# Performance work log

Measured on AMD Instinct MI355X. Metric: run time of the kernel, lower is better.

The kernel has to match this reference:

```python
import jax, jax.numpy as jnp
import numpy as np

N_NODES = 50000
N_RAND_EDGES = 800000  # plus N_NODES self-loop edges appended in setup
IN_FEATS, N_HIDDEN, N_CLASSES = 128, 64, 64


def setup_inputs() -> dict:
    key = jax.random.key(0)
    kf, ks, kd, k1, k2, k3 = jax.random.split(key, 6)
    features = jax.random.normal(kf, (N_NODES, IN_FEATS), dtype=jnp.float32)
    src = jax.random.randint(ks, (N_RAND_EDGES,), 0, N_NODES, dtype=jnp.int32)
    dst = jax.random.randint(kd, (N_RAND_EDGES,), 0, N_NODES, dtype=jnp.int32)
    # dgl.add_self_loop: append (i, i) for every node
    loop = jnp.arange(N_NODES, dtype=jnp.int32)
    src = jnp.concatenate([src, loop])
    dst = jnp.concatenate([dst, loop])

    def glorot(k, fan_in, fan_out):
        lim = jnp.sqrt(6.0 / (fan_in + fan_out)).astype(jnp.float32)
        return jax.random.uniform(k, (fan_in, fan_out), jnp.float32, -lim, lim)

    return {
        "features": features, "src": src, "dst": dst,
        "W1": glorot(k1, IN_FEATS, N_HIDDEN), "b1": jnp.zeros((N_HIDDEN,), jnp.float32),
        "W2": glorot(k2, N_HIDDEN, N_HIDDEN), "b2": jnp.zeros((N_HIDDEN,), jnp.float32),
        "W3": glorot(k3, N_HIDDEN, N_CLASSES), "b3": jnp.zeros((N_CLASSES,), jnp.float32),
    }


def _graph_conv(x, W, b, src, dst, norm_src_e, norm_dst_n, n_nodes):
    """DGL GraphConv, norm='both': D_dst^{-1/2} A D_src^{-1/2} X W + b, then relu."""
    if W.shape[0] > W.shape[1]:  # mult by W first when it shrinks the feature dim
        x = x @ W
        m = x[src] * norm_src_e[:, None]                      # [E, out]
        h = jax.ops.segment_sum(m, dst, num_segments=n_nodes)  # [N, out]
        h = h * norm_dst_n[:, None]
    else:
        m = x[src] * norm_src_e[:, None]                      # [E, in]
        h = jax.ops.segment_sum(m, dst, num_segments=n_nodes)  # [N, in]
        h = (h * norm_dst_n[:, None]) @ W
    return jax.nn.relu(h + b)


def reference(features, src, dst, W1, b1, W2, b2, W3, b3):
    n = features.shape[0]
    ones = jnp.ones(src.shape[0], dtype=features.dtype)
    out_deg = jax.ops.segment_sum(ones, src, num_segments=n)
    in_deg = jax.ops.segment_sum(ones, dst, num_segments=n)
    norm_out = jnp.where(out_deg > 0, jax.lax.rsqrt(jnp.maximum(out_deg, 1.0)), 0.0)
    norm_in = jnp.where(in_deg > 0, jax.lax.rsqrt(jnp.maximum(in_deg, 1.0)), 0.0)
    norm_src_e = norm_out[src]  # per-edge source normalization

    h1 = _graph_conv(features, W1, b1, src, dst, norm_src_e, norm_in, n)
    h2 = _graph_conv(h1, W2, b2, src, dst, norm_src_e, norm_in, n)
    h3 = _graph_conv(h2, W3, b3, src, dst, norm_src_e, norm_in, n)
    # JumpingKnowledge mode='max': elementwise max over stacked layer outputs
    return jnp.max(jnp.stack([h1, h2, h3], axis=0), axis=0)
```

## Files before the change

kernel.cpp:

```cpp
#include <hip/hip_runtime.h>

typedef _Float16 h16;
typedef __attribute__((ext_vector_type(4))) _Float16 half4;
typedef __attribute__((ext_vector_type(8))) _Float16 half8;
typedef __attribute__((ext_vector_type(8))) float float8;

#define RANGES 4
#define PPR    64
#define HTHREADS 1024
#define BINS   12800
#define HALF   (BINS / 2)
#define HWORDS (BINS)
#define NSEG   100
#define NFILL  (RANGES * PPR)
#define SMEMB  (BINS * 4 + 512)

__global__ __launch_bounds__(HTHREADS) void hist_kernel(const int* __restrict__ src,
                                                        const int* __restrict__ dst,
                                                        int* __restrict__ partial, int E) {
  __shared__ int h[HWORDS];
  const int r = blockIdx.x >> 6;
  const int c = blockIdx.x & 63;
  for (int i = threadIdx.x; i < HWORDS; i += HTHREADS) h[i] = 0;
  __syncthreads();
  const int lo = r * BINS;
  const int chunk = (E + PPR - 1) / PPR;
  const int e0 = c * chunk;
  const int e1 = min(E, e0 + chunk);
  for (int e = e0 + threadIdx.x; e < e1; e += HTHREADS) {
    int s = src[e] - lo;
    if ((unsigned)s < (unsigned)BINS) atomicAdd(&h[s >> 1], 1 << ((s & 1) * 16));
    int d = dst[e] - lo;
    if ((unsigned)d < (unsigned)BINS) atomicAdd(&h[HALF + (d >> 1)], 1 << ((d & 1) * 16));
  }
  __syncthreads();
  int* op = partial + (size_t)blockIdx.x * HWORDS;
  for (int i = threadIdx.x; i < HWORDS; i += HTHREADS) op[i] = h[i];
}

__global__ __launch_bounds__(256) void reduce_norm_scan1(
    int* __restrict__ partial, float* __restrict__ nout, float* __restrict__ nin,
    int* __restrict__ rowptr, int* __restrict__ bsums, int N) {
  __shared__ int s[256];
  const int j = blockIdx.x * 256 + threadIdx.x;
  const int r = j / HALF;
  const int w = j % HALF;
  int* base = partial + (size_t)(r * PPR) * HWORDS;
  int sumO = 0, runI = 0;
#pragma unroll 8
  for (int p = 0; p < PPR; ++p) {
    sumO += base[(size_t)p * HWORDS + w];
    int vI = base[(size_t)p * HWORDS + HALF + w];
    base[(size_t)p * HWORDS + HALF + w] = runI;
    runI += vI;
  }
  const int od0 = sumO & 0xFFFF, od1 = (sumO >> 16) & 0xFFFF;
  const int id0 = runI & 0xFFFF, id1 = (runI >> 16) & 0xFFFF;
  const int n0 = 2 * j, n1 = n0 + 1;
  if (n0 < N) {
    nout[n0] = od0 > 0 ? rsqrtf((float)od0) : 0.f;
    nin[n0]  = id0 > 0 ? rsqrtf((float)id0) : 0.f;
  }
  if (n1 < N) {
    nout[n1] = od1 > 0 ? rsqrtf((float)od1) : 0.f;
    nin[n1]  = id1 > 0 ? rsqrtf((float)id1) : 0.f;
  }
  const int local = id0 + id1;
  int v = local;
  s[threadIdx.x] = v;
  __syncthreads();
#pragma unroll
  for (int off = 1; off < 256; off <<= 1) {
    int tv = 0;
    if (threadIdx.x >= off) tv = s[threadIdx.x - off];
    __syncthreads();
    if (threadIdx.x >= off) s[threadIdx.x] += tv;
    __syncthreads();
  }
  const int excl = s[threadIdx.x] - v;
  if (n0 < N) rowptr[n0] = excl;
  if (n1 < N) rowptr[n1] = excl + id0;
  if (threadIdx.x == 255) bsums[blockIdx.x] = s[255];
}

__global__ __launch_bounds__(HTHREADS) void fill_gemm_kernel(
    const int* __restrict__ src, const int* __restrict__ dst,
    const int* __restrict__ rowptr, const int* __restrict__ bsums,
    const int* __restrict__ partial, int* __restrict__ rowptr_abs,
    unsigned short* __restrict__ csr,
    const float* __restrict__ feat, const float* __restrict__ W1,
    const float* __restrict__ nout, half4* __restrict__ bufAh,
    int N, int E) {
  __shared__ __align__(16) char smem[SMEMB];
  const int tid = threadIdx.x;

  if (blockIdx.x < NFILL) {
    int* cur = (int*)smem;
    int* top = (int*)(smem + BINS * 4);
    const int r = blockIdx.x & 3;
    const int c = blockIdx.x >> 2;
    if (tid < 128) top[tid] = (tid < NSEG) ? bsums[tid] : 0;
    __syncthreads();
#pragma unroll
    for (int off = 1; off < 128; off <<= 1) {
      int v = 0;
      if (tid < 128 && tid >= off) v = top[tid - off];
      __syncthreads();
      if (tid < 128 && tid >= off) top[tid] += v;
      __syncthreads();
    }
    const int lo = r * BINS;
    const int* pf = partial + (size_t)(r * PPR + c) * HWORDS + HALF;
    for (int n = tid; n < BINS; n += HTHREADS) {
      int g = lo + n;
      int rp = 0;
      if (g < N) {
        int seg = g >> 9;
        rp = rowptr[g] + (seg ? top[seg - 1] : 0);
        if (c == 0) rowptr_abs[g] = rp;
      }
      int pw = pf[n >> 1];
      cur[n] = rp + ((pw >> ((n & 1) * 16)) & 0xFFFF);
    }
    if (blockIdx.x == 0 && tid == 0) rowptr_abs[N] = E;
    __syncthreads();
    const int chunk = (E + PPR - 1) / PPR;
    const int e0 = c * chunk;
    const int e1 = min(E, e0 + chunk);
    for (int e = e0 + tid; e < e1; e += HTHREADS) {
      int d = dst[e] - lo;
      if ((unsigned)d < (unsigned)BINS) {
        int pos = atomicAdd(&cur[d], 1);
        csr[pos] = (unsigned short)src[e];
      }
    }
  } else {
    float* sA = (float*)smem;
    float* sB = (float*)(smem + 128 * 68 * 4);
    const int tile = blockIdx.x - NFILL;
    const int row0 = tile << 7;
    const int ry = tid >> 4;
    const int tx = tid & 15;
    const int r0 = 2 * ry, r1 = r0 + 1;
    float4 acc0 = make_float4(0.f, 0.f, 0.f, 0.f);
    float4 acc1 = make_float4(0.f, 0.f, 0.f, 0.f);
#pragma unroll
    for (int kc = 0; kc < 2; ++kc) {
      __syncthreads();
      for (int i = tid * 4; i < 128 * 64; i += HTHREADS * 4) {
        int rr = i >> 6, cc = i & 63;
        int gr = row0 + rr;
        float4 v = make_float4(0.f, 0.f, 0.f, 0.f);
        if (gr < N) v = *reinterpret_cast<const float4*>(feat + (size_t)gr * 128 + kc * 64 + cc);
        *reinterpret_cast<float4*>(sA + rr * 68 + cc) = v;
      }
      {
        int i = tid * 4;
        int rr = i >> 6, cc = i & 63;
        *reinterpret_cast<float4*>(sB + rr * 64 + cc) =
            *reinterpret_cast<const float4*>(W1 + (size_t)(kc * 64 + rr) * 64 + cc);
      }
      __syncthreads();
#pragma unroll 8
      for (int k = 0; k < 64; ++k) {
        float a0 = sA[r0 * 68 + k], a1 = sA[r1 * 68 + k];
        float4 b = *reinterpret_cast<float4*>(sB + k * 64 + tx * 4);
        acc0.x += a0 * b.x; acc0.y += a0 * b.y; acc0.z += a0 * b.z; acc0.w += a0 * b.w;
        acc1.x += a1 * b.x; acc1.y += a1 * b.y; acc1.z += a1 * b.z; acc1.w += a1 * b.w;
      }
    }
#pragma unroll
    for (int rr = 0; rr < 2; ++rr) {
      const int gr = row0 + (rr ? r1 : r0);
      if (gr >= N) continue;
      float4 v = rr ? acc1 : acc0;
      float no = nout[gr];
      half4 hv;
      hv.x = (h16)(v.x * no); hv.y = (h16)(v.y * no);
      hv.z = (h16)(v.z * no); hv.w = (h16)(v.w * no);
      bufAh[(size_t)gr * 16 + tx] = hv;
    }
  }
}

__device__ __forceinline__ float8 gather_row(const int* __restrict__ rowptr,
                                             const unsigned short* __restrict__ csr,
                                             const half8* __restrict__ xv,
                                             int node, int lane) {
  const int b = rowptr[node], e = rowptr[node + 1];
  float8 a0 = 0.f, a1 = 0.f, a2 = 0.f, a3 = 0.f;
  int i = b;
  for (; i + 8 <= e; i += 8) {
    int s0 = csr[i + 0], s1 = csr[i + 1], s2 = csr[i + 2], s3 = csr[i + 3];
    int s4 = csr[i + 4], s5 = csr[i + 5], s6 = csr[i + 6], s7 = csr[i + 7];
    half8 v0 = xv[(size_t)s0 * 8 + lane];
    half8 v1 = xv[(size_t)s1 * 8 + lane];
    half8 v2 = xv[(size_t)s2 * 8 + lane];
    half8 v3 = xv[(size_t)s3 * 8 + lane];
    half8 v4 = xv[(size_t)s4 * 8 + lane];
    half8 v5 = xv[(size_t)s5 * 8 + lane];
    half8 v6 = xv[(size_t)s6 * 8 + lane];
    half8 v7 = xv[(size_t)s7 * 8 + lane];
#pragma unroll
    for (int j = 0; j < 8; ++j) {
      a0[j] += (float)v0[j]; a1[j] += (float)v1[j];
      a2[j] += (float)v2[j]; a3[j] += (float)v3[j];
      a0[j] += (float)v4[j]; a1[j] += (float)v5[j];
      a2[j] += (float)v6[j]; a3[j] += (float)v7[j];
    }
  }
  for (; i + 4 <= e; i += 4) {
    int s0 = csr[i + 0], s1 = csr[i + 1], s2 = csr[i + 2], s3 = csr[i + 3];
    half8 v0 = xv[(size_t)s0 * 8 + lane];
    half8 v1 = xv[(size_t)s1 * 8 + lane];
    half8 v2 = xv[(size_t)s2 * 8 + lane];
    half8 v3 = xv[(size_t)s3 * 8 + lane];
#pragma unroll
    for (int j = 0; j < 8; ++j) {
      a0[j] += (float)v0[j]; a1[j] += (float)v1[j];
      a2[j] += (float)v2[j]; a3[j] += (float)v3[j];
    }
  }
  for (; i < e; ++i) {
    int s = csr[i];
    half8 v = xv[(size_t)s * 8 + lane];
#pragma unroll
    for (int j = 0; j < 8; ++j) a0[j] += (float)v[j];
  }
#pragma unroll
  for (int j = 0; j < 8; ++j) a0[j] = (a0[j] + a1[j]) + (a2[j] + a3[j]);
  return a0;
}

__global__ __launch_bounds__(512) void agg1_kernel(
    const int* __restrict__ rowptr, const unsigned short* __restrict__ csr,
    const h16* __restrict__ x, const float* __restrict__ nin,
    const float* __restrict__ bias, const float* __restrict__ nout,
    half8* __restrict__ y, float* __restrict__ out, int N) {
  int t = blockIdx.x * 512 + threadIdx.x;
  int node = t >> 3;
  if (node >= N) return;
  int lane = t & 7;
  float8 acc = gather_row(rowptr, csr, reinterpret_cast<const half8*>(x), node, lane);
  const float s = nin[node];
  const float no = nout[node];
  float8 h;
  half8 hv;
#pragma unroll
  for (int j = 0; j < 8; ++j) {
    h[j] = fmaxf(acc[j] * s + bias[lane * 8 + j], 0.f);
    hv[j] = (h16)(h[j] * no);
  }
  size_t off = (size_t)node * 64 + lane * 8;
  *reinterpret_cast<float4*>(out + off)     = make_float4(h[0], h[1], h[2], h[3]);
  *reinterpret_cast<float4*>(out + off + 4) = make_float4(h[4], h[5], h[6], h[7]);
  y[(size_t)node * 8 + lane] = hv;
}

template <bool WRITEC>
__global__ __launch_bounds__(512) void fused_layer(
    const int* __restrict__ rowptr, const unsigned short* __restrict__ csr,
    const h16* __restrict__ x, const float* __restrict__ W,
    const float* __restrict__ nin, const float* __restrict__ bias,
    const float* __restrict__ nout,
    half4* __restrict__ C, float* __restrict__ out, int N) {
  __shared__ float sA[64][68];
  __shared__ float sB[64][64];
  const int t = threadIdx.x;
  const int row0 = blockIdx.x * 64;

  for (int i = t * 4; i < 64 * 64; i += 512 * 4)
    *reinterpret_cast<float4*>(&sB[0][0] + i) = *reinterpret_cast<const float4*>(W + i);

  {
    const int node = t >> 3, lane = t & 7;
    const int g = row0 + node;
    float8 acc = 0.f;
    float s = 0.f;
    if (g < N) {
      acc = gather_row(rowptr, csr, reinterpret_cast<const half8*>(x), g, lane);
      s = nin[g];
    }
    *reinterpret_cast<float4*>(&sA[node][lane * 8]) =
        make_float4(acc[0] * s, acc[1] * s, acc[2] * s, acc[3] * s);
    *reinterpret_cast<float4*>(&sA[node][lane * 8 + 4]) =
        make_float4(acc[4] * s, acc[5] * s, acc[6] * s, acc[7] * s);
  }
  __syncthreads();

  const int tx = t & 15;
  const int ry = t >> 4;
  const int r0 = 2 * ry, r1 = r0 + 1;
  float4 a0 = make_float4(0.f, 0.f, 0.f, 0.f);
  float4 a1 = make_float4(0.f, 0.f, 0.f, 0.f);
#pragma unroll 8
  for (int k = 0; k < 64; ++k) {
    float x0 = sA[r0][k], x1 = sA[r1][k];
    float4 b = *reinterpret_cast<float4*>(&sB[k][tx * 4]);
    a0.x += x0 * b.x; a0.y += x0 * b.y; a0.z += x0 * b.z; a0.w += x0 * b.w;
    a1.x += x1 * b.x; a1.y += x1 * b.y; a1.z += x1 * b.z; a1.w += x1 * b.w;
  }

  const float4 bb = *reinterpret_cast<const float4*>(bias + tx * 4);
#pragma unroll
  for (int rr = 0; rr < 2; ++rr) {
    const int gr = row0 + (rr ? r1 : r0);
    if (gr >= N) continue;
    float4 v = rr ? a1 : a0;
    v.x = fmaxf(v.x + bb.x, 0.f);
    v.y = fmaxf(v.y + bb.y, 0.f);
    v.z = fmaxf(v.z + bb.z, 0.f);
    v.w = fmaxf(v.w + bb.w, 0.f);
    size_t off = (size_t)gr * 64 + tx * 4;
    float4 o = *reinterpret_cast<float4*>(out + off);
    o.x = fmaxf(o.x, v.x);
    o.y = fmaxf(o.y, v.y);
    o.z = fmaxf(o.z, v.z);
    o.w = fmaxf(o.w, v.w);
    *reinterpret_cast<float4*>(out + off) = o;
    if (WRITEC) {
      float no = nout[gr];
      half4 hv;
      hv.x = (h16)(v.x * no); hv.y = (h16)(v.y * no);
      hv.z = (h16)(v.z * no); hv.w = (h16)(v.w * no);
      C[(size_t)gr * 16 + tx] = hv;
    }
  }
}

extern "C" void kernel_launch(void* const* d_in, const int* in_sizes, int n_in,
                              void* d_out, int out_size, void* d_ws, size_t ws_size,
                              hipStream_t stream) {
  const float* feat = (const float*)d_in[0];
  const int* src    = (const int*)d_in[1];
  const int* dst    = (const int*)d_in[2];
  const float* W1   = (const float*)d_in[3];
  const float* b1   = (const float*)d_in[4];
  const float* W2   = (const float*)d_in[5];
  const float* b2   = (const float*)d_in[6];
  const float* W3   = (const float*)d_in[7];
  const float* b3   = (const float*)d_in[8];
  float* out = (float*)d_out;

  const int N = in_sizes[0] / 128;
  const int E = in_sizes[1];

  char* p = (char*)d_ws;
  float* nout       = (float*)p;     p += (size_t)N * 4;
  float* nin        = (float*)p;     p += (size_t)N * 4;
  int*   rowptr     = (int*)p;       p += ((size_t)N + 8) * 4;
  int*   rowptr_abs = (int*)p;       p += ((size_t)N + 8) * 4;
  int*   bsums      = (int*)p;       p += 1024 * 4;
  unsigned short* csr = (unsigned short*)p;  p += (((size_t)E + 8) & ~7) * 2;
  p = (char*)(((uintptr_t)p + 15) & ~(uintptr_t)15);
  h16*   bufAh = (h16*)p;            p += (size_t)N * 64 * 2;
  h16*   bufBh = (h16*)p;            p += (size_t)N * 64 * 2;
  p = (char*)(((uintptr_t)p + 15) & ~(uintptr_t)15);
  int*   partial = (int*)p;          p += (size_t)RANGES * PPR * HWORDS * 4;

  const int ngemm = (N + 127) / 128;

  hist_kernel<<<NFILL, HTHREADS, 0, stream>>>(src, dst, partial, E);
  reduce_norm_scan1<<<NSEG, 256, 0, stream>>>(partial, nout, nin, rowptr, bsums, N);
  fill_gemm_kernel<<<NFILL + ngemm, HTHREADS, 0, stream>>>(
      src, dst, rowptr, bsums, partial, rowptr_abs, csr,
      feat, W1, nout, (half4*)bufAh, N, E);

  const int gemm_blocks = (N + 63) / 64;
  const int agg1_blocks = (int)(((size_t)N * 8 + 511) / 512);

  agg1_kernel<<<agg1_blocks, 512, 0, stream>>>(rowptr_abs, csr, bufAh, nin, b1, nout,
                                               (half8*)bufBh, out, N);
  fused_layer<true><<<gemm_blocks, 512, 0, stream>>>(rowptr_abs, csr, bufBh, W2, nin, b2, nout,
                                                     (half4*)bufAh, out, N);
  fused_layer<false><<<gemm_blocks, 512, 0, stream>>>(rowptr_abs, csr, bufAh, W3, nin, b3, nullptr,
                                                      nullptr, out, N);
}
```

Before: 147.3 us.

## Split feature tables into column halves and decouple gather from GEMM

Feature tables are stored as two column halves (32 features each, in separate N-sized planes). Aggregation kernels gather one half at a time, with block indices interleaved so that each half's gathered working set (3.2 MB) is more likely to stay cache-resident. The fused gather+GEMM layers are split into separate aggregation and GEMM kernels, with the aggregate written to an intermediate fp16 buffer. This adds two launches and extra global traffic for the intermediate in exchange for better cache locality on the random gathers.

After: 151.7 us. 3.0% more time.

```diff
diff --git a/kernel.cpp b/kernel.cpp
--- a/kernel.cpp
+++ b/kernel.cpp
@@ -89,7 +89,7 @@
     const int* __restrict__ partial, int* __restrict__ rowptr_abs,
     unsigned short* __restrict__ csr,
     const float* __restrict__ feat, const float* __restrict__ W1,
-    const float* __restrict__ nout, half4* __restrict__ bufAh,
+    const float* __restrict__ nout, half4* __restrict__ tabA,
     int N, int E) {
   __shared__ __align__(16) char smem[SMEMB];
   const int tid = threadIdx.x;
@@ -178,29 +178,29 @@
       half4 hv;
       hv.x = (h16)(v.x * no); hv.y = (h16)(v.y * no);
       hv.z = (h16)(v.z * no); hv.w = (h16)(v.w * no);
-      bufAh[(size_t)gr * 16 + tx] = hv;
-    }
-  }
-}
-
-__device__ __forceinline__ float8 gather_row(const int* __restrict__ rowptr,
-                                             const unsigned short* __restrict__ csr,
-                                             const half8* __restrict__ xv,
-                                             int node, int lane) {
+      tabA[((size_t)(tx >> 3) * N + gr) * 8 + (tx & 7)] = hv;
+    }
+  }
+}
+
+__device__ __forceinline__ float8 gather32(const int* __restrict__ rowptr,
+                                           const unsigned short* __restrict__ csr,
+                                           const half8* __restrict__ xv,
+                                           int node, int lane) {
   const int b = rowptr[node], e = rowptr[node + 1];
   float8 a0 = 0.f, a1 = 0.f, a2 = 0.f, a3 = 0.f;
   int i = b;
   for (; i + 8 <= e; i += 8) {
     int s0 = csr[i + 0], s1 = csr[i + 1], s2 = csr[i + 2], s3 = csr[i + 3];
     int s4 = csr[i + 4], s5 = csr[i + 5], s6 = csr[i + 6], s7 = csr[i + 7];
-    half8 v0 = xv[(size_t)s0 * 8 + lane];
-    half8 v1 = xv[(size_t)s1 * 8 + lane];
-    half8 v2 = xv[(size_t)s2 * 8 + lane];
-    half8 v3 = xv[(size_t)s3 * 8 + lane];
-    half8 v4 = xv[(size_t)s4 * 8 + lane];
-    half8 v5 = xv[(size_t)s5 * 8 + lane];
-    half8 v6 = xv[(size_t)s6 * 8 + lane];
-    half8 v7 = xv[(size_t)s7 * 8 + lane];
+    half8 v0 = xv[(size_t)s0 * 4 + lane];
+    half8 v1 = xv[(size_t)s1 * 4 + lane];
+    half8 v2 = xv[(size_t)s2 * 4 + lane];
+    half8 v3 = xv[(size_t)s3 * 4 + lane];
+    half8 v4 = xv[(size_t)s4 * 4 + lane];
+    half8 v5 = xv[(size_t)s5 * 4 + lane];
+    half8 v6 = xv[(size_t)s6 * 4 + lane];
+    half8 v7 = xv[(size_t)s7 * 4 + lane];
 #pragma unroll
     for (int j = 0; j < 8; ++j) {
       a0[j] += (float)v0[j]; a1[j] += (float)v1[j];
@@ -211,10 +211,10 @@
   }
   for (; i + 4 <= e; i += 4) {
     int s0 = csr[i + 0], s1 = csr[i + 1], s2 = csr[i + 2], s3 = csr[i + 3];
-    half8 v0 = xv[(size_t)s0 * 8 + lane];
-    half8 v1 = xv[(size_t)s1 * 8 + lane];
-    half8 v2 = xv[(size_t)s2 * 8 + lane];
-    half8 v3 = xv[(size_t)s3 * 8 + lane];
+    half8 v0 = xv[(size_t)s0 * 4 + lane];
+    half8 v1 = xv[(size_t)s1 * 4 + lane];
+    half8 v2 = xv[(size_t)s2 * 4 + lane];
+    half8 v3 = xv[(size_t)s3 * 4 + lane];
 #pragma unroll
     for (int j = 0; j < 8; ++j) {
       a0[j] += (float)v0[j]; a1[j] += (float)v1[j];
@@ -223,7 +223,7 @@
   }
   for (; i < e; ++i) {
     int s = csr[i];
-    half8 v = xv[(size_t)s * 8 + lane];
+    half8 v = xv[(size_t)s * 4 + lane];
 #pragma unroll
     for (int j = 0; j < 8; ++j) a0[j] += (float)v[j];
   }
@@ -232,38 +232,47 @@
   return a0;
 }
 
-__global__ __launch_bounds__(512) void agg1_kernel(
+template <bool L1>
+__global__ __launch_bounds__(1024) void aggS_kernel(
     const int* __restrict__ rowptr, const unsigned short* __restrict__ csr,
-    const h16* __restrict__ x, const float* __restrict__ nin,
+    const half8* __restrict__ xsplit, const float* __restrict__ nin,
     const float* __restrict__ bias, const float* __restrict__ nout,
-    half8* __restrict__ y, float* __restrict__ out, int N) {
-  int t = blockIdx.x * 512 + threadIdx.x;
-  int node = t >> 3;
+    half8* __restrict__ ysplit, float* __restrict__ out, int N) {
+  const int bid = blockIdx.x, tid = threadIdx.x;
+  const int h = (bid & 7) >> 2;
+  const int c = (bid >> 3) * 4 + (bid & 3);
+  const int node = c * 256 + (tid >> 2);
   if (node >= N) return;
-  int lane = t & 7;
-  float8 acc = gather_row(rowptr, csr, reinterpret_cast<const half8*>(x), node, lane);
-  const float s = nin[node];
-  const float no = nout[node];
-  float8 h;
-  half8 hv;
-#pragma unroll
-  for (int j = 0; j < 8; ++j) {
-    h[j] = fmaxf(acc[j] * s + bias[lane * 8 + j], 0.f);
-    hv[j] = (h16)(h[j] * no);
-  }
-  size_t off = (size_t)node * 64 + lane * 8;
-  *reinterpret_cast<float4*>(out + off)     = make_float4(h[0], h[1], h[2], h[3]);
-  *reinterpret_cast<float4*>(out + off + 4) = make_float4(h[4], h[5], h[6], h[7]);
-  y[(size_t)node * 8 + lane] = hv;
+  const int lane = tid & 3;
+  const half8* xv = xsplit + (size_t)h * N * 4;
+  float8 acc = gather32(rowptr, csr, xv, node, lane);
+  const float sN = nin[node];
+  if (L1) {
+    const float no = nout[node];
+    float8 hh;
+    half8 hv;
+#pragma unroll
+    for (int j = 0; j < 8; ++j) {
+      hh[j] = fmaxf(acc[j] * sN + bias[h * 32 + lane * 8 + j], 0.f);
+      hv[j] = (h16)(hh[j] * no);
+    }
+    size_t off = (size_t)node * 64 + h * 32 + lane * 8;
+    *reinterpret_cast<float4*>(out + off)     = make_float4(hh[0], hh[1], hh[2], hh[3]);
+    *reinterpret_cast<float4*>(out + off + 4) = make_float4(hh[4], hh[5], hh[6], hh[7]);
+    ysplit[((size_t)h * N + node) * 4 + lane] = hv;
+  } else {
+    half8 hv;
+#pragma unroll
+    for (int j = 0; j < 8; ++j) hv[j] = (h16)(acc[j] * sN);
+    ysplit[((size_t)h * N + node) * 4 + lane] = hv;
+  }
 }
 
 template <bool WRITEC>
-__global__ __launch_bounds__(512) void fused_layer(
-    const int* __restrict__ rowptr, const unsigned short* __restrict__ csr,
-    const h16* __restrict__ x, const float* __restrict__ W,
-    const float* __restrict__ nin, const float* __restrict__ bias,
-    const float* __restrict__ nout,
-    half4* __restrict__ C, float* __restrict__ out, int N) {
+__global__ __launch_bounds__(512) void gemmS_kernel(
+    const half8* __restrict__ A, const float* __restrict__ W,
+    const float* __restrict__ bias, const float* __restrict__ nout,
+    half4* __restrict__ Cs, float* __restrict__ out, int N) {
   __shared__ float sA[64][68];
   __shared__ float sB[64][64];
   const int t = threadIdx.x;
@@ -273,18 +282,17 @@
     *reinterpret_cast<float4*>(&sB[0][0] + i) = *reinterpret_cast<const float4*>(W + i);
 
   {
-    const int node = t >> 3, lane = t & 7;
+    const int node = t >> 3, l8 = t & 7;
+    const int h = l8 >> 2, lane = l8 & 3;
     const int g = row0 + node;
-    float8 acc = 0.f;
-    float s = 0.f;
+    float8 v = 0.f;
     if (g < N) {
-      acc = gather_row(rowptr, csr, reinterpret_cast<const half8*>(x), g, lane);
-      s = nin[g];
-    }
-    *reinterpret_cast<float4*>(&sA[node][lane * 8]) =
-        make_float4(acc[0] * s, acc[1] * s, acc[2] * s, acc[3] * s);
-    *reinterpret_cast<float4*>(&sA[node][lane * 8 + 4]) =
-        make_float4(acc[4] * s, acc[5] * s, acc[6] * s, acc[7] * s);
+      half8 hv = A[((size_t)h * N + g) * 4 + lane];
+#pragma unroll
+      for (int j = 0; j < 8; ++j) v[j] = (float)hv[j];
+    }
+    *reinterpret_cast<float4*>(&sA[node][l8 * 8])     = make_float4(v[0], v[1], v[2], v[3]);
+    *reinterpret_cast<float4*>(&sA[node][l8 * 8 + 4]) = make_float4(v[4], v[5], v[6], v[7]);
   }
   __syncthreads();
 
@@ -323,7 +331,7 @@
       half4 hv;
       hv.x = (h16)(v.x * no); hv.y = (h16)(v.y * no);
       hv.z = (h16)(v.z * no); hv.w = (h16)(v.w * no);
-      C[(size_t)gr * 16 + tx] = hv;
+      Cs[((size_t)(tx >> 3) * N + gr) * 8 + (tx & 7)] = hv;
     }
   }
 }
@@ -353,26 +361,33 @@
   int*   bsums      = (int*)p;       p += 1024 * 4;
   unsigned short* csr = (unsigned short*)p;  p += (((size_t)E + 8) & ~7) * 2;
   p = (char*)(((uintptr_t)p + 15) & ~(uintptr_t)15);
-  h16*   bufAh = (h16*)p;            p += (size_t)N * 64 * 2;
-  h16*   bufBh = (h16*)p;            p += (size_t)N * 64 * 2;
+  h16* tabA = (h16*)p;               p += (size_t)N * 64 * 2;
+  h16* tabB = (h16*)p;               p += (size_t)N * 64 * 2;
+  h16* aggT = (h16*)p;               p += (size_t)N * 64 * 2;
   p = (char*)(((uintptr_t)p + 15) & ~(uintptr_t)15);
-  int*   partial = (int*)p;          p += (size_t)RANGES * PPR * HWORDS * 4;
+  int* partial = (int*)p;            p += (size_t)RANGES * PPR * HWORDS * 4;
 
   const int ngemm = (N + 127) / 128;
+  const int chunks = (N + 255) / 256;
+  const int aggs_blocks = ((chunks + 3) / 4) * 8;
+  const int gemms_blocks = (N + 63) / 64;
 
   hist_kernel<<<NFILL, HTHREADS, 0, stream>>>(src, dst, partial, E);
   reduce_norm_scan1<<<NSEG, 256, 0, stream>>>(partial, nout, nin, rowptr, bsums, N);
   fill_gemm_kernel<<<NFILL + ngemm, HTHREADS, 0, stream>>>(
       src, dst, rowptr, bsums, partial, rowptr_abs, csr,
-      feat, W1, nout, (half4*)bufAh, N, E);
-
-  const int gemm_blocks = (N + 63) / 64;
-  const int agg1_blocks = (int)(((size_t)N * 8 + 511) / 512);
-
-  agg1_kernel<<<agg1_blocks, 512, 0, stream>>>(rowptr_abs, csr, bufAh, nin, b1, nout,
-                                               (half8*)bufBh, out, N);
-  fused_layer<true><<<gemm_blocks, 512, 0, stream>>>(rowptr_abs, csr, bufBh, W2, nin, b2, nout,
-                                                     (half4*)bufAh, out, N);
-  fused_layer<false><<<gemm_blocks, 512, 0, stream>>>(rowptr_abs, csr, bufAh, W3, nin, b3, nullptr,
-                                                      nullptr, out, N);
-}
+      feat, W1, nout, (half4*)tabA, N, E);
+
+  aggS_kernel<true><<<aggs_blocks, 1024, 0, stream>>>(
+      rowptr_abs, csr, (const half8*)tabA, nin, b1, nout, (half8*)tabB, out, N);
+
+  aggS_kernel<false><<<aggs_blocks, 1024, 0, stream>>>(
+      rowptr_abs, csr, (const half8*)tabB, nin, nullptr, nullptr, (half8*)aggT, nullptr, N);
+  gemmS_kernel<true><<<gemms_blocks, 512, 0, stream>>>(
+      (const half8*)aggT, W2, b2, nout, (half4*)tabA, out, N);
+
+  aggS_kernel<false><<<aggs_blocks, 1024, 0, stream>>>(
+      rowptr_abs, csr, (const half8*)tabA, nin, nullptr, nullptr, (half8*)aggT, nullptr, N);
+  gemmS_kernel<false><<<gemms_blocks, 512, 0, stream>>>(
+      (const half8*)aggT, W3, b3, nullptr, nullptr, out, N);
+}
```
